# Kernel tuning notes

Measured on AMD Instinct MI355X. Metric: run time of the kernel, lower is better.

## Reference

```python
import jax, jax.numpy as jnp
import numpy as np

K = 5  # up_kernel

def bilinear(x, hw):
    # torch F.interpolate bilinear, align_corners=False (half-pixel), no antialias
    return jax.image.resize(x, x.shape[:2] + hw, method='linear', antialias=False)

def nearest2x(x):
    return jnp.repeat(jnp.repeat(x, 2, axis=2), 2, axis=3)

def conv3x3(x, w, b):
    y = jax.lax.conv_general_dilated(x, w, (1, 1), [(1, 1), (1, 1)],
                                     dimension_numbers=('NCHW', 'OIHW', 'NCHW'))
    return y + b[None, :, None, None]

def carafe(x, mask):
    # x: [N,C,H,W]; mask: [N,K*K,H,W] softmax-normalized. scale_factor=1, up_group=1.
    N, C, H, W = x.shape
    r = K // 2
    xp = jnp.pad(x, ((0, 0), (0, 0), (r, r), (r, r)))
    out = jnp.zeros_like(x)
    idx = 0
    for di in range(K):
        for dj in range(K):
            out = out + xp[:, :, di:di + H, dj:dj + W] * mask[:, idx:idx + 1]
            idx += 1
    return out

def setup_inputs() -> dict:
    key = jax.random.key(0)
    ks = jax.random.split(key, 6)
    feat = jax.random.normal(ks[0], (1, 32, 96, 96), jnp.float32)
    seg = jax.random.normal(ks[1], (1, 19, 96, 96), jnp.float32)
    img = jax.random.uniform(ks[2], (1, 3, 384, 384), jnp.float32)
    w_enc0 = jax.random.normal(ks[3], (25, 35, 3, 3), jnp.float32) * 0.05
    b_enc0 = jnp.zeros((25,), jnp.float32)
    w_enc1 = jax.random.normal(ks[4], (25, 35, 3, 3), jnp.float32) * 0.05
    b_enc1 = jnp.zeros((25,), jnp.float32)
    return {'feat': feat, 'seg': seg, 'img': img,
            'w_enc0': w_enc0, 'b_enc0': b_enc0, 'w_enc1': w_enc1, 'b_enc1': b_enc1}

def reference(feat, seg, img, w_enc0, b_enc0, w_enc1, b_enc1):
    weights = [(w_enc0, b_enc0), (w_enc1, b_enc1)]
    for i in range(2):
        Hf, Wf = feat.shape[-2], feat.shape[-1]
        resized_img = bilinear(img, (2 * Hf, 2 * Wf))
        # high-boost filtering: img_hf = img - lowpass(img) + img
        lr = bilinear(resized_img, (Hf, Wf))
        lr = bilinear(lr, (2 * Hf, 2 * Wf))
        img_hf = 2.0 * resized_img - lr
        feat_up = nearest2x(feat)
        seg_up = nearest2x(seg)
        w, b = weights[i]
        mask = conv3x3(jnp.concatenate([feat_up, img_hf], axis=1), w, b)
        # kernel_normalizer: pixel_shuffle(1)=identity, softmax over the 25 kernel taps
        mask = jax.nn.softmax(mask, axis=1)
        seg = carafe(seg_up, mask)
        feat = carafe(feat_up, mask)
    return seg
```

## Files before the change

### kernel.cpp

```cpp
#include <hip/hip_runtime.h>


__global__ __launch_bounds__(256) void repack_kernel(
    const float* __restrict__ w0s, const float* __restrict__ w1s,
    float* __restrict__ W2a, float* __restrict__ wTha,
    float* __restrict__ W2b, float* __restrict__ wThb) {
  int i = blockIdx.x * 256 + threadIdx.x;
  const float* w; float* W2; float* wTh; int k = i;
  if (i < 13475) { w = w0s; W2 = W2a; wTh = wTha; }
  else { k = i - 13475; if (k >= 13475) return; w = w1s; W2 = W2b; wTh = wThb; }
  if (k < 12800) {
    int oc = k % 25; int j = k / 25;
    int src = j & 3; j >>= 2;
    int ic = j & 31; int p = j >> 5;
    int py = p >> 1, px = p & 1;
    int a = src >> 1, b = src & 1;
    float s = 0.f;
    for (int ky = 0; ky < 3; ++ky) {
      int rs = (py == 0) ? (ky >= 1) : (ky >= 2);
      if (rs != a) continue;
      for (int kx = 0; kx < 3; ++kx) {
        int cs = (px == 0) ? (kx >= 1) : (kx >= 2);
        if (cs != b) continue;
        s += w[oc * 315 + ic * 9 + ky * 3 + kx];
      }
    }
    W2[k] = s;
  } else {
    int kk = k - 12800;
    int oc = kk % 25; int j = kk / 25;
    int h = j % 3; int tap = j / 3;
    wTh[kk] = w[oc * 315 + (32 + h) * 9 + tap];
  }
}

__global__ __launch_bounds__(256) void down2_kernel(
    const float* __restrict__ in, float* __restrict__ out) {
  int idx = blockIdx.x * 256 + threadIdx.x;
  if (idx >= 3 * 192 * 192) return;
  int x = idx % 192; int t = idx / 192; int y = t % 192; int c = t / 192;
  const float* p = in + (c * 384 + 2 * y) * 384 + 2 * x;
  out[idx] = 0.25f * (p[0] + p[1] + p[384] + p[385]);
}

__global__ __launch_bounds__(256) void hf0_kernel(
    const float* __restrict__ I192, float* __restrict__ out) {
  int idx = blockIdx.x * 256 + threadIdx.x;
  if (idx >= 3 * 192 * 192) return;
  int x = idx % 192; int t = idx / 192; int y = t % 192; int c = t / 192;
  int m = y >> 1; int ya, yb; float wya, wyb;
  if ((y & 1) == 0) { ya = m - 1 < 0 ? 0 : m - 1; yb = m; wya = 0.25f; wyb = 0.75f; }
  else             { ya = m; yb = m + 1 > 95 ? 95 : m + 1; wya = 0.75f; wyb = 0.25f; }
  int n = x >> 1; int xa, xb; float wxa, wxb;
  if ((x & 1) == 0) { xa = n - 1 < 0 ? 0 : n - 1; xb = n; wxa = 0.25f; wxb = 0.75f; }
  else             { xa = n; xb = n + 1 > 95 ? 95 : n + 1; wxa = 0.75f; wxb = 0.25f; }
  const float* base = I192 + c * 192 * 192;
  auto I96v = [&](int mm, int nn) {
    const float* p = base + (2 * mm) * 192 + 2 * nn;
    return 0.25f * (p[0] + p[1] + p[192] + p[193]);
  };
  float up = wya * (wxa * I96v(ya, xa) + wxb * I96v(ya, xb))
           + wyb * (wxa * I96v(yb, xa) + wxb * I96v(yb, xb));
  out[idx] = 2.0f * base[y * 192 + x] - up;
}

__global__ __launch_bounds__(256) void highboost_kernel(
    const float* __restrict__ base, const float* __restrict__ lr,
    float* __restrict__ out) {
  const int H = 192, OW = 384;
  int idx = blockIdx.x * 256 + threadIdx.x;
  if (idx >= 3 * 384 * 384) return;
  int x = idx % OW; int t = idx / OW; int y = t % 384; int c = t / 384;
  int m = y >> 1; int ya, yb; float wya, wyb;
  if ((y & 1) == 0) { ya = m - 1 < 0 ? 0 : m - 1; yb = m; wya = 0.25f; wyb = 0.75f; }
  else             { ya = m; yb = m + 1 >= H ? H - 1 : m + 1; wya = 0.75f; wyb = 0.25f; }
  int n = x >> 1; int xa, xb; float wxa, wxb;
  if ((x & 1) == 0) { xa = n - 1 < 0 ? 0 : n - 1; xb = n; wxa = 0.25f; wxb = 0.75f; }
  else             { xa = n; xb = n + 1 >= H ? H - 1 : n + 1; wxa = 0.75f; wxb = 0.25f; }
  const float* p = lr + c * H * H;
  float up = wya * (wxa * p[ya * H + xa] + wxb * p[ya * H + xb])
           + wyb * (wxa * p[yb * H + xa] + wxb * p[yb * H + xb]);
  out[idx] = 2.0f * base[idx] - up;
}

__global__ __launch_bounds__(256, 4) void conv_softmax_kernel(
    const float* __restrict__ feat, const float* __restrict__ hf,
    const float* __restrict__ W2, const float* __restrict__ wTh,
    const float* __restrict__ b, float* __restrict__ CW,
    int Hf, int Wf) {
  const int OH = 2 * Hf, OW = 2 * Wf, Np = OH * OW, fp = Hf * Wf;
  __shared__ float sf[32 * 144];
  __shared__ float sh[3 * 408];
  const int t = threadIdx.x;
  const int TW = Wf >> 5;
  const int wg = ((blockIdx.x & 7) * (gridDim.x >> 3)) + (blockIdx.x >> 3);
  const int tx = wg % TW, ty = wg / TW;
  const int gx0 = tx << 5, gy0 = ty << 1;

  for (int i = t; i < 32 * 136; i += 256) {
    int ic = i / 136, rem = i - ic * 136;
    int r = rem / 34, c = rem - r * 34;
    int gr = gy0 - 1 + r, gc = gx0 - 1 + c;
    float v = 0.f;
    if ((unsigned)gr < (unsigned)Hf && (unsigned)gc < (unsigned)Wf)
      v = feat[ic * fp + gr * Wf + gc];
    sf[ic * 144 + r * 36 + c] = v;
  }
  for (int i = t; i < 3 * 396; i += 256) {
    int ch = i / 396, rem = i - ch * 396;
    int R = rem / 66, C = rem - R * 66;
    int gr = 2 * gy0 - 1 + R, gc = 2 * gx0 - 1 + C;
    float v = 0.f;
    if ((unsigned)gr < (unsigned)OH && (unsigned)gc < (unsigned)OW)
      v = hf[ch * Np + gr * OW + gc];
    sh[ch * 408 + R * 68 + C] = v;
  }
  __syncthreads();

  const int w = __builtin_amdgcn_readfirstlane(t >> 6);
  const int lane = t & 63;
  const int py = w >> 1, px = w & 1;
  const int ly = lane >> 5, lx = lane & 31;
  const int lr0 = ly + py;
  const int lc0 = lx + px;

  float acc[25];
#pragma unroll
  for (int oc = 0; oc < 25; ++oc) acc[oc] = b[oc];

  for (int ic = 0; ic < 32; ++ic) {
    const float* base = sf + ic * 144 + lr0 * 36 + lc0;
    float v00 = base[0], v01 = base[1], v10 = base[36], v11 = base[37];
    const float* wp = W2 + (size_t)((w * 32 + ic) * 4) * 25;
#pragma unroll
    for (int oc = 0; oc < 25; ++oc)
      acc[oc] += v00 * wp[oc] + v01 * wp[25 + oc] + v10 * wp[50 + oc] + v11 * wp[75 + oc];
  }
  {
    const int R0 = 2 * ly + py, C0 = 2 * lx + px;
#pragma unroll
    for (int ky = 0; ky < 3; ++ky)
#pragma unroll
      for (int kx = 0; kx < 3; ++kx)
#pragma unroll
        for (int ch = 0; ch < 3; ++ch) {
          float v = sh[ch * 408 + (R0 + ky) * 68 + (C0 + kx)];
          const float* wp = wTh + ((ky * 3 + kx) * 3 + ch) * 25;
#pragma unroll
          for (int oc = 0; oc < 25; ++oc) acc[oc] = fmaf(v, wp[oc], acc[oc]);
        }
  }

  const int y = 2 * (gy0 + ly) + py, x = 2 * (gx0 + lx) + px;
  float mx = acc[0];
#pragma unroll
  for (int oc = 1; oc < 25; ++oc) mx = fmaxf(mx, acc[oc]);
  float ssum = 0.f;
#pragma unroll
  for (int oc = 0; oc < 25; ++oc) { acc[oc] = __expf(acc[oc] - mx); ssum += acc[oc]; }
  float inv = 1.0f / ssum;

  bool vy[5], vx[5];
#pragma unroll
  for (int d = 0; d < 5; ++d) {
    vy[d] = (unsigned)(y + d - 2) < (unsigned)OH;
    vx[d] = (unsigned)(x + d - 2) < (unsigned)OW;
  }
  float rs[3][5];
  if (py == 0) {
#pragma unroll
    for (int dj = 0; dj < 5; ++dj) {
      float m0 = (vy[0] && vx[dj]) ? acc[0 + dj] : 0.f;
      float m1 = (vy[1] && vx[dj]) ? acc[5 + dj] : 0.f;
      float m2 = (vy[2] && vx[dj]) ? acc[10 + dj] : 0.f;
      float m3 = (vy[3] && vx[dj]) ? acc[15 + dj] : 0.f;
      float m4 = (vy[4] && vx[dj]) ? acc[20 + dj] : 0.f;
      rs[0][dj] = m0 + m1; rs[1][dj] = m2 + m3; rs[2][dj] = m4;
    }
  } else {
#pragma unroll
    for (int dj = 0; dj < 5; ++dj) {
      float m0 = (vy[0] && vx[dj]) ? acc[0 + dj] : 0.f;
      float m1 = (vy[1] && vx[dj]) ? acc[5 + dj] : 0.f;
      float m2 = (vy[2] && vx[dj]) ? acc[10 + dj] : 0.f;
      float m3 = (vy[3] && vx[dj]) ? acc[15 + dj] : 0.f;
      float m4 = (vy[4] && vx[dj]) ? acc[20 + dj] : 0.f;
      rs[0][dj] = m0; rs[1][dj] = m1 + m2; rs[2][dj] = m3 + m4;
    }
  }
  float cw[9];
#pragma unroll
  for (int r = 0; r < 3; ++r) {
    if (px == 0) {
      cw[r * 3 + 0] = rs[r][0] + rs[r][1];
      cw[r * 3 + 1] = rs[r][2] + rs[r][3];
      cw[r * 3 + 2] = rs[r][4];
    } else {
      cw[r * 3 + 0] = rs[r][0];
      cw[r * 3 + 1] = rs[r][1] + rs[r][2];
      cw[r * 3 + 2] = rs[r][3] + rs[r][4];
    }
  }
  const int pix = y * OW + x;
#pragma unroll
  for (int tap = 0; tap < 9; ++tap) CW[tap * Np + pix] = cw[tap] * inv;
}

__global__ __launch_bounds__(256) void carafe_kernel(
    const float* __restrict__ CW,
    const float* __restrict__ in0, float* __restrict__ out0, int C0,
    const float* __restrict__ in1, float* __restrict__ out1, int C1,
    int CS, int Hf, int Wf) {
  const int OW = 2 * Wf;
  const int Np = 4 * Hf * Wf;
  int pix = blockIdx.x * 256 + threadIdx.x;
  if (pix >= Np) return;
  int x = pix % OW, y = pix / OW;
  int ry0 = (y >> 1) - 1, rx0 = (x >> 1) - 1;
  int sy[3], sx[3];
#pragma unroll
  for (int i = 0; i < 3; ++i) {
    int v = ry0 + i; sy[i] = v < 0 ? 0 : (v >= Hf ? Hf - 1 : v);
    int u = rx0 + i; sx[i] = u < 0 ? 0 : (u >= Wf ? Wf - 1 : u);
  }
  float cw[9];
#pragma unroll
  for (int i = 0; i < 9; ++i) cw[i] = CW[i * Np + pix];
  const int fplane = Hf * Wf;
  int cbeg = blockIdx.y * CS;
  int cend = cbeg + CS; int Ct = C0 + C1; if (cend > Ct) cend = Ct;
  for (int c = cbeg; c < cend; ++c) {
    const float* p; float* q;
    if (c < C0) { p = in0 + c * fplane; q = out0 + c * Np; }
    else        { p = in1 + (c - C0) * fplane; q = out1 + (c - C0) * Np; }
    const float* r0 = p + sy[0] * Wf;
    const float* r1 = p + sy[1] * Wf;
    const float* r2 = p + sy[2] * Wf;
    float acc = cw[0] * r0[sx[0]] + cw[1] * r0[sx[1]] + cw[2] * r0[sx[2]]
              + cw[3] * r1[sx[0]] + cw[4] * r1[sx[1]] + cw[5] * r1[sx[2]]
              + cw[6] * r2[sx[0]] + cw[7] * r2[sx[1]] + cw[8] * r2[sx[2]];
    q[pix] = acc;
  }
}

extern "C" void kernel_launch(void* const* d_in, const int* in_sizes, int n_in,
                              void* d_out, int out_size, void* d_ws, size_t ws_size,
                              hipStream_t stream) {
  (void)in_sizes; (void)n_in; (void)out_size; (void)ws_size;
  const float* feat = (const float*)d_in[0];
  const float* seg  = (const float*)d_in[1];
  const float* img  = (const float*)d_in[2];
  const float* w0   = (const float*)d_in[3];
  const float* b0   = (const float*)d_in[4];
  const float* w1   = (const float*)d_in[5];
  const float* b1   = (const float*)d_in[6];
  float* out = (float*)d_out;

  float* ws   = (float*)d_ws;
  float* I192 = ws;
  float* HF   = I192 + 3 * 192 * 192;
  float* CWb  = HF   + 3 * 384 * 384;
  float* F1   = CWb  + 9 * 384 * 384;
  float* S1   = F1   + 32 * 192 * 192;
  float* W2_0 = S1   + 19 * 192 * 192;
  float* WTH0 = W2_0 + 12800;
  float* W2_1 = WTH0 + 675;
  float* WTH1 = W2_1 + 12800;

  repack_kernel<<<106, 256, 0, stream>>>(w0, w1, W2_0, WTH0, W2_1, WTH1);
  down2_kernel<<<432, 256, 0, stream>>>(img, I192);

  hf0_kernel<<<432, 256, 0, stream>>>(I192, HF);
  conv_softmax_kernel<<<48 * 3, 256, 0, stream>>>(
      feat, HF, W2_0, WTH0, b0, CWb, 96, 96);
  carafe_kernel<<<dim3(144, 3), 256, 0, stream>>>(
      CWb, seg, S1, 19, feat, F1, 32, 17, 96, 96);

  highboost_kernel<<<1728, 256, 0, stream>>>(img, I192, HF);
  conv_softmax_kernel<<<96 * 6, 256, 0, stream>>>(
      F1, HF, W2_1, WTH1, b1, CWb, 192, 192);
  carafe_kernel<<<dim3(576, 2), 256, 0, stream>>>(
      CWb, S1, out, 19, nullptr, nullptr, 0, 10, 192, 192);
}
```

Baseline: 184.9 us.

## Fuse carafe into conv-softmax kernel and fold image preprocessing into prep

Merges the carafe reassembly into the conv+softmax kernel so the nine per-pixel kernel weights stay in registers and the seg/feat tiles are read from shared memory. This removes the CW round trip through global memory. The high-boost image filtering is computed directly from the input image, inside the prep kernel for stage 0 and in the halo load for stage 1, which drops several launches and intermediate buffers. The cost is more shared memory per block (an added seg tile), recomputed bilinear work in the halo loads, and a launch_bounds occupancy hint that was removed.

```diff
diff --git a/kernel.cpp b/kernel.cpp
--- a/kernel.cpp
+++ b/kernel.cpp
@@ -1,95 +1,77 @@
 #include <hip/hip_runtime.h>
 
 
-__global__ __launch_bounds__(256) void repack_kernel(
+__global__ __launch_bounds__(256) void prep_kernel(
     const float* __restrict__ w0s, const float* __restrict__ w1s,
+    const float* __restrict__ img,
     float* __restrict__ W2a, float* __restrict__ wTha,
-    float* __restrict__ W2b, float* __restrict__ wThb) {
-  int i = blockIdx.x * 256 + threadIdx.x;
-  const float* w; float* W2; float* wTh; int k = i;
-  if (i < 13475) { w = w0s; W2 = W2a; wTh = wTha; }
-  else { k = i - 13475; if (k >= 13475) return; w = w1s; W2 = W2b; wTh = wThb; }
-  if (k < 12800) {
-    int oc = k % 25; int j = k / 25;
-    int src = j & 3; j >>= 2;
-    int ic = j & 31; int p = j >> 5;
-    int py = p >> 1, px = p & 1;
-    int a = src >> 1, b = src & 1;
-    float s = 0.f;
-    for (int ky = 0; ky < 3; ++ky) {
-      int rs = (py == 0) ? (ky >= 1) : (ky >= 2);
-      if (rs != a) continue;
-      for (int kx = 0; kx < 3; ++kx) {
-        int cs = (px == 0) ? (kx >= 1) : (kx >= 2);
-        if (cs != b) continue;
-        s += w[oc * 315 + ic * 9 + ky * 3 + kx];
+    float* __restrict__ W2b, float* __restrict__ wThb,
+    float* __restrict__ HF0) {
+  if (blockIdx.x < 106) {
+    int i = blockIdx.x * 256 + threadIdx.x;
+    const float* w; float* W2; float* wTh; int k = i;
+    if (i < 13475) { w = w0s; W2 = W2a; wTh = wTha; }
+    else { k = i - 13475; if (k >= 13475) return; w = w1s; W2 = W2b; wTh = wThb; }
+    if (k < 12800) {
+      int oc = k % 25; int j = k / 25;
+      int src = j & 3; j >>= 2;
+      int ic = j & 31; int p = j >> 5;
+      int py = p >> 1, px = p & 1;
+      int a = src >> 1, b = src & 1;
+      float s = 0.f;
+      for (int ky = 0; ky < 3; ++ky) {
+        int rs = (py == 0) ? (ky >= 1) : (ky >= 2);
+        if (rs != a) continue;
+        for (int kx = 0; kx < 3; ++kx) {
+          int cs = (px == 0) ? (kx >= 1) : (kx >= 2);
+          if (cs != b) continue;
+          s += w[oc * 315 + ic * 9 + ky * 3 + kx];
+        }
       }
-    }
-    W2[k] = s;
-  } else {
-    int kk = k - 12800;
-    int oc = kk % 25; int j = kk / 25;
-    int h = j % 3; int tap = j / 3;
-    wTh[kk] = w[oc * 315 + (32 + h) * 9 + tap];
-  }
-}
-
-__global__ __launch_bounds__(256) void down2_kernel(
-    const float* __restrict__ in, float* __restrict__ out) {
-  int idx = blockIdx.x * 256 + threadIdx.x;
+      W2[k] = s;
+    } else {
+      int kk = k - 12800;
+      int oc = kk % 25; int j = kk / 25;
+      int h = j % 3; int tap = j / 3;
+      wTh[kk] = w[oc * 315 + (32 + h) * 9 + tap];
+    }
+    return;
+  }
+  int idx = (blockIdx.x - 106) * 256 + threadIdx.x;
   if (idx >= 3 * 192 * 192) return;
-  int x = idx % 192; int t = idx / 192; int y = t % 192; int c = t / 192;
-  const float* p = in + (c * 384 + 2 * y) * 384 + 2 * x;
-  out[idx] = 0.25f * (p[0] + p[1] + p[384] + p[385]);
-}
-
-__global__ __launch_bounds__(256) void hf0_kernel(
-    const float* __restrict__ I192, float* __restrict__ out) {
-  int idx = blockIdx.x * 256 + threadIdx.x;
-  if (idx >= 3 * 192 * 192) return;
-  int x = idx % 192; int t = idx / 192; int y = t % 192; int c = t / 192;
+  int x = idx % 192; int t2 = idx / 192; int y = t2 % 192; int c = t2 / 192;
+  const float* ip = img + c * 147456;
   int m = y >> 1; int ya, yb; float wya, wyb;
   if ((y & 1) == 0) { ya = m - 1 < 0 ? 0 : m - 1; yb = m; wya = 0.25f; wyb = 0.75f; }
   else             { ya = m; yb = m + 1 > 95 ? 95 : m + 1; wya = 0.75f; wyb = 0.25f; }
   int n = x >> 1; int xa, xb; float wxa, wxb;
   if ((x & 1) == 0) { xa = n - 1 < 0 ? 0 : n - 1; xb = n; wxa = 0.25f; wxb = 0.75f; }
   else             { xa = n; xb = n + 1 > 95 ? 95 : n + 1; wxa = 0.75f; wxb = 0.25f; }
-  const float* base = I192 + c * 192 * 192;
   auto I96v = [&](int mm, int nn) {
-    const float* p = base + (2 * mm) * 192 + 2 * nn;
-    return 0.25f * (p[0] + p[1] + p[192] + p[193]);
+    const float* p = ip + (4 * mm) * 384 + 4 * nn;
+    float s = 0.f;
+#pragma unroll
+    for (int i = 0; i < 4; ++i) s += p[i * 384] + p[i * 384 + 1] + p[i * 384 + 2] + p[i * 384 + 3];
+    return s * 0.0625f;
   };
+  const float* q = ip + (2 * y) * 384 + 2 * x;
+  float i192 = 0.25f * (q[0] + q[1] + q[384] + q[385]);
   float up = wya * (wxa * I96v(ya, xa) + wxb * I96v(ya, xb))
            + wyb * (wxa * I96v(yb, xa) + wxb * I96v(yb, xb));
-  out[idx] = 2.0f * base[y * 192 + x] - up;
+  HF0[idx] = 2.0f * i192 - up;
 }
 
-__global__ __launch_bounds__(256) void highboost_kernel(
-    const float* __restrict__ base, const float* __restrict__ lr,
-    float* __restrict__ out) {
-  const int H = 192, OW = 384;
-  int idx = blockIdx.x * 256 + threadIdx.x;
-  if (idx >= 3 * 384 * 384) return;
-  int x = idx % OW; int t = idx / OW; int y = t % 384; int c = t / 384;
-  int m = y >> 1; int ya, yb; float wya, wyb;
-  if ((y & 1) == 0) { ya = m - 1 < 0 ? 0 : m - 1; yb = m; wya = 0.25f; wyb = 0.75f; }
-  else             { ya = m; yb = m + 1 >= H ? H - 1 : m + 1; wya = 0.75f; wyb = 0.25f; }
-  int n = x >> 1; int xa, xb; float wxa, wxb;
-  if ((x & 1) == 0) { xa = n - 1 < 0 ? 0 : n - 1; xb = n; wxa = 0.25f; wxb = 0.75f; }
-  else             { xa = n; xb = n + 1 >= H ? H - 1 : n + 1; wxa = 0.75f; wxb = 0.25f; }
-  const float* p = lr + c * H * H;
-  float up = wya * (wxa * p[ya * H + xa] + wxb * p[ya * H + xb])
-           + wyb * (wxa * p[yb * H + xa] + wxb * p[yb * H + xb]);
-  out[idx] = 2.0f * base[idx] - up;
-}
-
-__global__ __launch_bounds__(256, 4) void conv_softmax_kernel(
-    const float* __restrict__ feat, const float* __restrict__ hf,
+template <int MODE>
+__global__ __launch_bounds__(256) void fused_kernel(
+    const float* __restrict__ feat, const float* __restrict__ seg,
+    const float* __restrict__ img, const float* __restrict__ HF0,
     const float* __restrict__ W2, const float* __restrict__ wTh,
-    const float* __restrict__ b, float* __restrict__ CW,
+    const float* __restrict__ b,
+    float* __restrict__ outF, float* __restrict__ outS,
     int Hf, int Wf) {
   const int OH = 2 * Hf, OW = 2 * Wf, Np = OH * OW, fp = Hf * Wf;
   __shared__ float sf[32 * 144];
+  __shared__ float ss[19 * 144];
   __shared__ float sh[3 * 408];
   const int t = threadIdx.x;
   const int TW = Wf >> 5;
@@ -106,13 +88,40 @@
       v = feat[ic * fp + gr * Wf + gc];
     sf[ic * 144 + r * 36 + c] = v;
   }
+  for (int i = t; i < 19 * 136; i += 256) {
+    int sc = i / 136, rem = i - sc * 136;
+    int r = rem / 34, c = rem - r * 34;
+    int gr = gy0 - 1 + r, gc = gx0 - 1 + c;
+    float v = 0.f;
+    if ((unsigned)gr < (unsigned)Hf && (unsigned)gc < (unsigned)Wf)
+      v = seg[sc * fp + gr * Wf + gc];
+    ss[sc * 144 + r * 36 + c] = v;
+  }
   for (int i = t; i < 3 * 396; i += 256) {
     int ch = i / 396, rem = i - ch * 396;
     int R = rem / 66, C = rem - R * 66;
     int gr = 2 * gy0 - 1 + R, gc = 2 * gx0 - 1 + C;
     float v = 0.f;
-    if ((unsigned)gr < (unsigned)OH && (unsigned)gc < (unsigned)OW)
-      v = hf[ch * Np + gr * OW + gc];
+    if ((unsigned)gr < (unsigned)OH && (unsigned)gc < (unsigned)OW) {
+      if (MODE == 0) {
+        v = HF0[ch * 36864 + gr * 192 + gc];
+      } else {
+        const float* ip = img + ch * 147456;
+        int m = gr >> 1; int ya, yb; float wya, wyb;
+        if ((gr & 1) == 0) { ya = m - 1 < 0 ? 0 : m - 1; yb = m; wya = 0.25f; wyb = 0.75f; }
+        else               { ya = m; yb = m + 1 > 191 ? 191 : m + 1; wya = 0.75f; wyb = 0.25f; }
+        int n = gc >> 1; int xa, xb; float wxa, wxb;
+        if ((gc & 1) == 0) { xa = n - 1 < 0 ? 0 : n - 1; xb = n; wxa = 0.25f; wxb = 0.75f; }
+        else               { xa = n; xb = n + 1 > 191 ? 191 : n + 1; wxa = 0.75f; wxb = 0.25f; }
+        auto I192v = [&](int mm, int nn) {
+          const float* p = ip + (2 * mm) * 384 + 2 * nn;
+          return 0.25f * (p[0] + p[1] + p[384] + p[385]);
+        };
+        float up = wya * (wxa * I192v(ya, xa) + wxb * I192v(ya, xb))
+                 + wyb * (wxa * I192v(yb, xa) + wxb * I192v(yb, xb));
+        v = 2.0f * ip[gr * 384 + gc] - up;
+      }
+    }
     sh[ch * 408 + R * 68 + C] = v;
   }
   __syncthreads();
@@ -121,8 +130,7 @@
   const int lane = t & 63;
   const int py = w >> 1, px = w & 1;
   const int ly = lane >> 5, lx = lane & 31;
-  const int lr0 = ly + py;
-  const int lc0 = lx + px;
+  const int lr0 = ly + py, lc0 = lx + px;
 
   float acc[25];
 #pragma unroll
@@ -192,54 +200,32 @@
 #pragma unroll
   for (int r = 0; r < 3; ++r) {
     if (px == 0) {
-      cw[r * 3 + 0] = rs[r][0] + rs[r][1];
-      cw[r * 3 + 1] = rs[r][2] + rs[r][3];
-      cw[r * 3 + 2] = rs[r][4];
+      cw[r * 3 + 0] = (rs[r][0] + rs[r][1]) * inv;
+      cw[r * 3 + 1] = (rs[r][2] + rs[r][3]) * inv;
+      cw[r * 3 + 2] = rs[r][4] * inv;
     } else {
-      cw[r * 3 + 0] = rs[r][0];
-      cw[r * 3 + 1] = rs[r][1] + rs[r][2];
-      cw[r * 3 + 2] = rs[r][3] + rs[r][4];
-    }
-  }
+      cw[r * 3 + 0] = rs[r][0] * inv;
+      cw[r * 3 + 1] = (rs[r][1] + rs[r][2]) * inv;
+      cw[r * 3 + 2] = (rs[r][3] + rs[r][4]) * inv;
+    }
+  }
+
   const int pix = y * OW + x;
-#pragma unroll
-  for (int tap = 0; tap < 9; ++tap) CW[tap * Np + pix] = cw[tap] * inv;
-}
-
-__global__ __launch_bounds__(256) void carafe_kernel(
-    const float* __restrict__ CW,
-    const float* __restrict__ in0, float* __restrict__ out0, int C0,
-    const float* __restrict__ in1, float* __restrict__ out1, int C1,
-    int CS, int Hf, int Wf) {
-  const int OW = 2 * Wf;
-  const int Np = 4 * Hf * Wf;
-  int pix = blockIdx.x * 256 + threadIdx.x;
-  if (pix >= Np) return;
-  int x = pix % OW, y = pix / OW;
-  int ry0 = (y >> 1) - 1, rx0 = (x >> 1) - 1;
-  int sy[3], sx[3];
-#pragma unroll
-  for (int i = 0; i < 3; ++i) {
-    int v = ry0 + i; sy[i] = v < 0 ? 0 : (v >= Hf ? Hf - 1 : v);
-    int u = rx0 + i; sx[i] = u < 0 ? 0 : (u >= Wf ? Wf - 1 : u);
-  }
-  float cw[9];
-#pragma unroll
-  for (int i = 0; i < 9; ++i) cw[i] = CW[i * Np + pix];
-  const int fplane = Hf * Wf;
-  int cbeg = blockIdx.y * CS;
-  int cend = cbeg + CS; int Ct = C0 + C1; if (cend > Ct) cend = Ct;
-  for (int c = cbeg; c < cend; ++c) {
-    const float* p; float* q;
-    if (c < C0) { p = in0 + c * fplane; q = out0 + c * Np; }
-    else        { p = in1 + (c - C0) * fplane; q = out1 + (c - C0) * Np; }
-    const float* r0 = p + sy[0] * Wf;
-    const float* r1 = p + sy[1] * Wf;
-    const float* r2 = p + sy[2] * Wf;
-    float acc = cw[0] * r0[sx[0]] + cw[1] * r0[sx[1]] + cw[2] * r0[sx[2]]
-              + cw[3] * r1[sx[0]] + cw[4] * r1[sx[1]] + cw[5] * r1[sx[2]]
-              + cw[6] * r2[sx[0]] + cw[7] * r2[sx[1]] + cw[8] * r2[sx[2]];
-    q[pix] = acc;
+  for (int c = 0; c < 19; ++c) {
+    const float* p = ss + c * 144 + ly * 36 + lx;
+    float a = cw[0] * p[0]  + cw[1] * p[1]  + cw[2] * p[2]
+            + cw[3] * p[36] + cw[4] * p[37] + cw[5] * p[38]
+            + cw[6] * p[72] + cw[7] * p[73] + cw[8] * p[74];
+    outS[c * Np + pix] = a;
+  }
+  if (MODE == 0) {
+    for (int c = 0; c < 32; ++c) {
+      const float* p = sf + c * 144 + ly * 36 + lx;
+      float a = cw[0] * p[0]  + cw[1] * p[1]  + cw[2] * p[2]
+              + cw[3] * p[36] + cw[4] * p[37] + cw[5] * p[38]
+              + cw[6] * p[72] + cw[7] * p[73] + cw[8] * p[74];
+      outF[c * Np + pix] = a;
+    }
   }
 }
 
@@ -257,28 +243,19 @@
   float* out = (float*)d_out;
 
   float* ws   = (float*)d_ws;
-  float* I192 = ws;
-  float* HF   = I192 + 3 * 192 * 192;
-  float* CWb  = HF   + 3 * 384 * 384;
-  float* F1   = CWb  + 9 * 384 * 384;
+  float* HF0  = ws;
+  float* F1   = HF0  + 3 * 192 * 192;
   float* S1   = F1   + 32 * 192 * 192;
   float* W2_0 = S1   + 19 * 192 * 192;
   float* WTH0 = W2_0 + 12800;
   float* W2_1 = WTH0 + 675;
   float* WTH1 = W2_1 + 12800;
 
-  repack_kernel<<<106, 256, 0, stream>>>(w0, w1, W2_0, WTH0, W2_1, WTH1);
-  down2_kernel<<<432, 256, 0, stream>>>(img, I192);
-
-  hf0_kernel<<<432, 256, 0, stream>>>(I192, HF);
-  conv_softmax_kernel<<<48 * 3, 256, 0, stream>>>(
-      feat, HF, W2_0, WTH0, b0, CWb, 96, 96);
-  carafe_kernel<<<dim3(144, 3), 256, 0, stream>>>(
-      CWb, seg, S1, 19, feat, F1, 32, 17, 96, 96);
-
-  highboost_kernel<<<1728, 256, 0, stream>>>(img, I192, HF);
-  conv_softmax_kernel<<<96 * 6, 256, 0, stream>>>(
-      F1, HF, W2_1, WTH1, b1, CWb, 192, 192);
-  carafe_kernel<<<dim3(576, 2), 256, 0, stream>>>(
-      CWb, S1, out, 19, nullptr, nullptr, 0, 10, 192, 192);
+  prep_kernel<<<538, 256, 0, stream>>>(w0, w1, img, W2_0, WTH0, W2_1, WTH1, HF0);
+
+  fused_kernel<0><<<48 * 3, 256, 0, stream>>>(
+      feat, seg, img, HF0, W2_0, WTH0, b0, F1, S1, 96, 96);
+
+  fused_kernel<1><<<96 * 6, 256, 0, stream>>>(
+      F1, S1, img, nullptr, W2_1, WTH1, b1, nullptr, out, 192, 192);
 }
```

Result: faster. 163.6 us (-11.5%).
